# Optimization experiments

Measured on AMD Instinct MI355X. Metric: run time of the kernel, lower is better.

Reference implementation:

```python
import jax, jax.numpy as jnp
import numpy as np

B = 32
NODES = [200000, 1024, 256, 32]
CH = [1, 32, 64, 128]
EDGES = [2048000, 262144, 8192]
NCLS = 10


def _wn(V, g):
    # PyTorch weight_norm (dim=0): each output row rescaled to norm g[o]
    return g[:, None] * V / jnp.linalg.norm(V, axis=1, keepdims=True)


def _fgl(x, src, dst, n_out, W, b):
    # x: (B, C_in, N_in); sparse random-adjacency downsample then channel mix
    xt = jnp.moveaxis(x, 2, 0)                                   # (N_in, B, C_in)
    gathered = xt[src]                                           # (E, B, C_in)
    pooled = jax.ops.segment_sum(gathered, dst, num_segments=n_out)  # (N_out, B, C_in)
    return jnp.einsum('nbc,oc->bon', pooled, W) + b[None, :, None]   # (B, C_out, N_out)


def setup_inputs() -> dict:
    key = jax.random.key(0)
    ks = jax.random.split(key, 20)
    d = {}
    d['x'] = jax.random.normal(ks[0], (B, NODES[0]), jnp.float32)
    for i in range(3):
        e = EDGES[i]
        n_in, n_out = NODES[i], NODES[i + 1]
        d[f'edge_src{i}'] = jax.random.randint(ks[1 + 2 * i], (e,), 0, n_in, jnp.int32)
        d[f'edge_dst{i}'] = jnp.sort(jax.random.randint(ks[2 + 2 * i], (e,), 0, n_out, jnp.int32))
    for i in range(3):
        cin, cout = CH[i], CH[i + 1]
        d[f'V{i}'] = jax.random.normal(ks[7 + 3 * i], (cout, cin), jnp.float32) * 0.1
        d[f'g{i}'] = jnp.ones((cout,), jnp.float32)
        d[f'b{i}'] = jnp.zeros((cout,), jnp.float32)
    d['Vfc'] = jax.random.normal(ks[16], (NCLS, CH[-1] * NODES[-1]), jnp.float32) * 0.02
    d['gfc'] = jnp.ones((NCLS,), jnp.float32)
    d['bfc'] = jnp.zeros((NCLS,), jnp.float32)
    return d


def reference(x, edge_src0, edge_dst0, edge_src1, edge_dst1, edge_src2, edge_dst2,
              V0, g0, b0, V1, g1, b1, V2, g2, b2, Vfc, gfc, bfc):
    z = x[:, None, :]                                            # (B, 1, N_in)
    z = _fgl(z, edge_src0, edge_dst0, NODES[1], _wn(V0, g0), b0)  # (B, 32, 1024)
    z = _fgl(z, edge_src1, edge_dst1, NODES[2], _wn(V1, g1), b1)  # (B, 64, 256)
    z = _fgl(z, edge_src2, edge_dst2, NODES[3], _wn(V2, g2), b2)  # (B, 128, 32)
    flat = z.reshape(z.shape[0], -1)                             # (B, 4096)
    return flat @ _wn(Vfc, gfc).T + bfc                          # (B, NCLS)
```

## Files before the change

### kernel.cpp

```cpp
#include <hip/hip_runtime.h>
#include <math.h>

#define N0 200000
#define N1 1024
#define N2 256
#define N3 32
#define NE0 2048000
#define NE1 262144
#define NE2 8192
#define BATCH 32
#define NCLS 10
#define NB 4
#define SRC_PER_B 50000
#define TBLOCKS 1563
#define PREBLOCKS (N1 + TBLOCKS)

typedef _Float16 h2 __attribute__((ext_vector_type(2)));
typedef _Float16 h8 __attribute__((ext_vector_type(8)));

__device__ __forceinline__ int lower_bound_i(const int* __restrict__ a, int n, int key) {
    int lo = 0, hi = n;
    while (lo < hi) {
        int mid = (lo + hi) >> 1;
        if (a[mid] < key) lo = mid + 1; else hi = mid;
    }
    return lo;
}

__device__ __forceinline__ int wave_lower_bound(const int* __restrict__ a,
                                                int n, int key, int lane) {
    int lo = 0, hi = n;
    while (lo < hi) {
        int range = hi - lo;
        int step = (range + 63) >> 6;
        int p = lo + lane * step;
        bool ok = (p < hi) && (a[p] < key);
        unsigned long long m = __ballot(ok);
        if (m == 0ull) break;
        int L = 63 - __builtin_clzll(m);
        int nlo = lo + L * step + 1;
        int nhi = lo + (L + 1) * step;
        hi = (nhi < hi) ? nhi : hi;
        lo = nlo;
    }
    return lo;
}

__global__ __launch_bounds__(256) void k_pre(const float* __restrict__ x,
                                             h2* __restrict__ xt,
                                             const int* __restrict__ src,
                                             const int* __restrict__ dst,
                                             int* __restrict__ esrc,
                                             int* __restrict__ bstart) {
    const int i = blockIdx.x;
    const int tid = threadIdx.x;
    if (i >= N1) {
        const int t = i - N1;
        __shared__ float tile[32][129];
        const int col0 = t * 128;
        #pragma unroll
        for (int pass = 0; pass < 4; ++pass) {
            int row = (tid >> 5) + 8 * pass;
            int j4 = (tid & 31) * 4;
            int col = col0 + j4;
            if (col < N0) {
                const float4 v = *reinterpret_cast<const float4*>(&x[row * N0 + col]);
                tile[row][j4]     = v.x;
                tile[row][j4 + 1] = v.y;
                tile[row][j4 + 2] = v.z;
                tile[row][j4 + 3] = v.w;
            }
        }
        __syncthreads();
        h8* xt8 = reinterpret_cast<h8*>(xt);
        #pragma unroll
        for (int k = 0; k < 2; ++k) {
            int cl = (tid >> 2) + 64 * k;
            int col = col0 + cl;
            int c4 = tid & 3;
            if (col < N0) {
                h8 v;
                #pragma unroll
                for (int ii = 0; ii < 8; ++ii)
                    v[ii] = (_Float16)tile[8 * c4 + ii][cl];
                xt8[col * 4 + c4] = v;
            }
        }
        return;
    }
    const int n = i;
    const int wave = tid >> 6, lane = tid & 63;
    __shared__ int sB[2];
    if (wave < 2) {
        int r = wave_lower_bound(dst, NE0, n + wave, lane);
        if (lane == 0) sB[wave] = r;
    }
    __syncthreads();
    const int e0 = sB[0];
    const int e1 = sB[1];
    const int len = e1 - e0;
    const int q0 = e0 + (len * wave) / 4;
    const int q1 = e0 + (len * (wave + 1)) / 4;
    __shared__ int wcnt[4][NB];
    __shared__ int wbase[4][NB];

    int c0 = 0, c1 = 0, c2 = 0, c3 = 0;
    for (int base = q0; base < q1; base += 64) {
        int e = base + lane;
        int b = -1;
        if (e < q1) b = src[e] / SRC_PER_B;
        c0 += __popcll(__ballot(b == 0));
        c1 += __popcll(__ballot(b == 1));
        c2 += __popcll(__ballot(b == 2));
        c3 += __popcll(__ballot(b == 3));
    }
    if (lane == 0) { wcnt[wave][0] = c0; wcnt[wave][1] = c1; wcnt[wave][2] = c2; wcnt[wave][3] = c3; }
    __syncthreads();
    if (tid == 0) {
        int acc = e0;
        #pragma unroll
        for (int b = 0; b < NB; ++b) {
            bstart[n * (NB + 1) + b] = acc;
            #pragma unroll
            for (int w = 0; w < 4; ++w) { wbase[w][b] = acc; acc += wcnt[w][b]; }
        }
        bstart[n * (NB + 1) + NB] = acc;
    }
    __syncthreads();

    int u0 = wbase[wave][0], u1 = wbase[wave][1], u2 = wbase[wave][2], u3 = wbase[wave][3];
    for (int base = q0; base < q1; base += 64) {
        int e = base + lane;
        int s = 0, b = -1;
        if (e < q1) { s = src[e]; b = s / SRC_PER_B; }
        unsigned long long m0 = __ballot(b == 0);
        unsigned long long m1 = __ballot(b == 1);
        unsigned long long m2 = __ballot(b == 2);
        unsigned long long m3 = __ballot(b == 3);
        unsigned long long lt = (1ull << lane) - 1ull;
        if (b == 0)      esrc[u0 + __popcll(m0 & lt)] = s;
        else if (b == 1) esrc[u1 + __popcll(m1 & lt)] = s;
        else if (b == 2) esrc[u2 + __popcll(m2 & lt)] = s;
        else if (b == 3) esrc[u3 + __popcll(m3 & lt)] = s;
        u0 += __popcll(m0); u1 += __popcll(m1); u2 += __popcll(m2); u3 += __popcll(m3);
    }
}

__global__ __launch_bounds__(128) void k_gather0s(const h8* __restrict__ table,
                                                  const int* __restrict__ esrc,
                                                  const int* __restrict__ bstart,
                                                  _Float16* __restrict__ p0p) {
    const int b = blockIdx.x & (NB - 1);
    const int n = blockIdx.x >> 2;
    const int q0 = bstart[n * (NB + 1) + b];
    const int q1 = bstart[n * (NB + 1) + b + 1];
    const int tid = threadIdx.x;
    const int b4 = tid & 3;
    const int g  = tid >> 2;
    float acc[8] = {0.f, 0.f, 0.f, 0.f, 0.f, 0.f, 0.f, 0.f};
    int e = q0 + g;
    for (; e + 96 < q1; e += 128) {
        int s0 = esrc[e];
        int s1 = esrc[e + 32];
        int s2 = esrc[e + 64];
        int s3 = esrc[e + 96];
        h8 v0 = table[s0 * 4 + b4];
        h8 v1 = table[s1 * 4 + b4];
        h8 v2 = table[s2 * 4 + b4];
        h8 v3 = table[s3 * 4 + b4];
        #pragma unroll
        for (int i = 0; i < 8; ++i)
            acc[i] += (float)v0[i] + (float)v1[i] + (float)v2[i] + (float)v3[i];
    }
    for (; e < q1; e += 32) {
        int s = esrc[e];
        h8 v = table[s * 4 + b4];
        #pragma unroll
        for (int i = 0; i < 8; ++i) acc[i] += (float)v[i];
    }
    __shared__ float red[32][33];
    #pragma unroll
    for (int i = 0; i < 8; ++i) red[g][b4 * 8 + i] = acc[i];
    __syncthreads();
    #pragma unroll
    for (int s = 16; s >= 1; s >>= 1) {
        if (g < s) {
            #pragma unroll
            for (int i = 0; i < 8; ++i)
                red[g][b4 * 8 + i] += red[g + s][b4 * 8 + i];
        }
        __syncthreads();
    }
    if (tid < 32) p0p[(b * N1 + n) * 32 + tid] = (_Float16)red[0][tid];
}

__global__ __launch_bounds__(256) void k_gather1w(
    const h8* __restrict__ p0p, const int* __restrict__ src,
    const int* __restrict__ dst, _Float16* __restrict__ out_h,
    float* __restrict__ cnt_out,
    const float* __restrict__ V0, const float* __restrict__ g0, const float* __restrict__ b0,
    const float* __restrict__ V1, const float* __restrict__ g1, const float* __restrict__ b1,
    const float* __restrict__ V2, const float* __restrict__ g2, const float* __restrict__ b2,
    const float* __restrict__ Vfc, const float* __restrict__ gfc,
    float* __restrict__ M_, float* __restrict__ Q2_, float* __restrict__ R2_,
    float* __restrict__ B4_) {
    const int tid = threadIdx.x;
    if (blockIdx.x < N2) {
        const int n = blockIdx.x;
        const int e0 = lower_bound_i(dst, NE1, n);
        const int e1 = lower_bound_i(dst, NE1, n + 1);
        const int b4 = tid & 3;
        const int g  = tid >> 2;
        float acc[8] = {0.f, 0.f, 0.f, 0.f, 0.f, 0.f, 0.f, 0.f};
        for (int e = e0 + g; e < e1; e += 64) {
            int s = src[e];
            h8 v0 = p0p[0 * N1 * 4 + s * 4 + b4];
            h8 v1 = p0p[1 * N1 * 4 + s * 4 + b4];
            h8 v2 = p0p[2 * N1 * 4 + s * 4 + b4];
            h8 v3 = p0p[3 * N1 * 4 + s * 4 + b4];
            #pragma unroll
            for (int i = 0; i < 8; ++i)
                acc[i] += ((float)v0[i] + (float)v1[i]) + ((float)v2[i] + (float)v3[i]);
        }
        __shared__ float red[64][33];
        #pragma unroll
        for (int i = 0; i < 8; ++i) red[g][b4 * 8 + i] = acc[i];
        __syncthreads();
        #pragma unroll
        for (int s = 32; s >= 1; s >>= 1) {
            if (g < s) {
                #pragma unroll
                for (int i = 0; i < 8; ++i)
                    red[g][b4 * 8 + i] += red[g + s][b4 * 8 + i];
            }
            __syncthreads();
        }
        if (tid < 32) out_h[n * 32 + tid] = (_Float16)red[0][tid];
        else if (tid == 32) cnt_out[n] = (float)(e1 - e0);
        return;
    }
    const int k = blockIdx.x - N2;
    __shared__ float w0[32], u[64], v[64], p[128], q[128], r[128];
    __shared__ float redA[8][32], redB[8][32], redC[8][32], redD[8][32];
    __shared__ float nnred[4];
    __shared__ float scale_s;

    if (tid < 32) {
        float val = V0[tid];
        w0[tid] = g0[tid] * val / fabsf(val);
    }
    __syncthreads();
    if (tid < 64) {
        float nn = 0.f;
        #pragma unroll
        for (int c = 0; c < 32; ++c) { float t = V1[tid * 32 + c]; nn += t * t; }
        float inv = g1[tid] * rsqrtf(nn);
        float su = 0.f, sv = 0.f;
        #pragma unroll
        for (int c = 0; c < 32; ++c) {
            float w = V1[tid * 32 + c] * inv;
            su += w * w0[c]; sv += w * b0[c];
        }
        u[tid] = su; v[tid] = sv;
    }
    __syncthreads();
    if (tid < 128) {
        float nn = 0.f;
        #pragma unroll
        for (int c = 0; c < 64; ++c) { float t = V2[tid * 64 + c]; nn += t * t; }
        float inv = g2[tid] * rsqrtf(nn);
        float sp = 0.f, sq = 0.f, sr = 0.f;
        #pragma unroll
        for (int c = 0; c < 64; ++c) {
            float w = V2[tid * 64 + c] * inv;
            sp += w * u[c]; sq += w * v[c]; sr += w * b1[c];
        }
        p[tid] = sp; q[tid] = sq; r[tid] = sr;
    }
    __syncthreads();

    const int n3 = tid & 31, og = tid >> 5;
    float nn = 0.f, mk = 0.f, mq = 0.f, mr = 0.f, mb = 0.f;
    #pragma unroll
    for (int i = 0; i < 16; ++i) {
        int o = og + 8 * i;
        float w = Vfc[k * 4096 + tid + 256 * i];
        nn += w * w;
        mk += w * p[o]; mq += w * q[o]; mr += w * r[o]; mb += w * b2[o];
    }
    #pragma unroll
    for (int off = 32; off; off >>= 1) nn += __shfl_xor(nn, off);
    if ((tid & 63) == 0) nnred[tid >> 6] = nn;
    redA[og][n3] = mk; redB[og][n3] = mq; redC[og][n3] = mr; redD[og][n3] = mb;
    __syncthreads();
    if (tid == 0) {
        float s = nnred[0] + nnred[1] + nnred[2] + nnred[3];
        scale_s = gfc[k] * rsqrtf(s);
    }
    __syncthreads();
    if (tid < 32) {
        float smk = 0.f, smq = 0.f, smr = 0.f, smb = 0.f;
        #pragma unroll
        for (int i = 0; i < 8; ++i) {
            smk += redA[i][tid]; smq += redB[i][tid];
            smr += redC[i][tid]; smb += redD[i][tid];
        }
        float scale = scale_s;
        M_[k * 32 + tid]  = scale * smk;
        Q2_[k * 32 + tid] = scale * smq;
        R2_[k * 32 + tid] = scale * smr;
        float bs = scale * smb;
        #pragma unroll
        for (int off = 16; off; off >>= 1) bs += __shfl_xor(bs, off);
        if (tid == 0) B4_[k] = bs;
    }
}

__global__ __launch_bounds__(256) void k_gather2(const h8* __restrict__ table,
                                                 const int* __restrict__ src,
                                                 const int* __restrict__ dst,
                                                 const float* __restrict__ cnt_in,
                                                 float* __restrict__ out_f,
                                                 float* __restrict__ cnt_out,
                                                 float* __restrict__ t_out) {
    const int n = blockIdx.x;
    const int e0 = lower_bound_i(dst, NE2, n);
    const int e1 = lower_bound_i(dst, NE2, n + 1);
    const int tid = threadIdx.x;
    const int b4 = tid & 3;
    const int g  = tid >> 2;
    float acc[8] = {0.f, 0.f, 0.f, 0.f, 0.f, 0.f, 0.f, 0.f};
    float tacc = 0.f;
    for (int e = e0 + g; e < e1; e += 64) {
        int s = src[e];
        h8 v = table[s * 4 + b4];
        #pragma unroll
        for (int i = 0; i < 8; ++i) acc[i] += (float)v[i];
        if (b4 == 0) tacc += cnt_in[s];
    }
    __shared__ float red[64][33];
    __shared__ float tred[64];
    #pragma unroll
    for (int i = 0; i < 8; ++i) red[g][b4 * 8 + i] = acc[i];
    if (b4 == 0) tred[g] = tacc;
    __syncthreads();
    #pragma unroll
    for (int s = 32; s >= 1; s >>= 1) {
        if (g < s) {
            #pragma unroll
            for (int i = 0; i < 8; ++i)
                red[g][b4 * 8 + i] += red[g + s][b4 * 8 + i];
            if (b4 == 0) tred[g] += tred[g + s];
        }
        __syncthreads();
    }
    if (tid < 32) out_f[n * 32 + tid] = red[0][tid];
    else if (tid == 32) cnt_out[n] = (float)(e1 - e0);
    else if (tid == 33) t_out[n] = tred[0];
}

__global__ __launch_bounds__(64) void k_final(const float* __restrict__ M_,
                                              const float* __restrict__ Q2_,
                                              const float* __restrict__ R2_,
                                              const float* __restrict__ B4_,
                                              const float* __restrict__ bfc,
                                              const float* __restrict__ S2,
                                              const float* __restrict__ T2,
                                              const float* __restrict__ cnt2,
                                              float* __restrict__ out) {
    const int k = blockIdx.x;
    const int tid = threadIdx.x;
    __shared__ float Kc_s;
    float kc = 0.f;
    if (tid < 32)
        kc = Q2_[k * 32 + tid] * T2[tid] + R2_[k * 32 + tid] * cnt2[tid];
    #pragma unroll
    for (int off = 16; off; off >>= 1) kc += __shfl_xor(kc, off);
    if (tid == 0) Kc_s = kc + B4_[k] + bfc[k];
    __syncthreads();
    if (tid < 32) {
        int b = tid;
        float s = 0.f;
        #pragma unroll
        for (int n = 0; n < 32; ++n) s += M_[k * 32 + n] * S2[n * 32 + b];
        out[b * NCLS + k] = s + Kc_s;
    }
}

extern "C" void kernel_launch(void* const* d_in, const int* in_sizes, int n_in,
                              void* d_out, int out_size, void* d_ws, size_t ws_size,
                              hipStream_t stream) {
    const float* x   = (const float*)d_in[0];
    const int* src0  = (const int*)d_in[1];
    const int* dst0  = (const int*)d_in[2];
    const int* src1  = (const int*)d_in[3];
    const int* dst1  = (const int*)d_in[4];
    const int* src2  = (const int*)d_in[5];
    const int* dst2  = (const int*)d_in[6];
    const float* V0  = (const float*)d_in[7];
    const float* g0  = (const float*)d_in[8];
    const float* b0  = (const float*)d_in[9];
    const float* V1  = (const float*)d_in[10];
    const float* g1  = (const float*)d_in[11];
    const float* b1  = (const float*)d_in[12];
    const float* V2  = (const float*)d_in[13];
    const float* g2  = (const float*)d_in[14];
    const float* b2  = (const float*)d_in[15];
    const float* Vfc = (const float*)d_in[16];
    const float* gfc = (const float*)d_in[17];
    const float* bfc = (const float*)d_in[18];

    char* ws = (char*)d_ws;
    _Float16* xt   = (_Float16*)(ws);
    int* esrc      = (int*)(ws + 12800000);
    int* bstart    = (int*)(ws + 20992000);
    _Float16* P0p  = (_Float16*)(ws + 21012480);
    _Float16* S1h  = (_Float16*)(ws + 21274624);
    float* cnt1    = (float*)(ws + 21291008);
    float* S2      = (float*)(ws + 21292032);
    float* T2      = (float*)(ws + 21296128);
    float* cnt2    = (float*)(ws + 21296256);
    float* M_      = (float*)(ws + 21296384);
    float* Q2_     = (float*)(ws + 21297664);
    float* R2_     = (float*)(ws + 21298944);
    float* B4_     = (float*)(ws + 21300224);

    k_pre<<<PREBLOCKS, 256, 0, stream>>>(x, (h2*)xt, src0, dst0, esrc, bstart);
    k_gather0s<<<N1 * NB, 128, 0, stream>>>((const h8*)xt, esrc, bstart,
                                            (_Float16*)P0p);
    k_gather1w<<<N2 + NCLS, 256, 0, stream>>>((const h8*)P0p, src1, dst1,
                                              S1h, cnt1,
                                              V0, g0, b0, V1, g1, b1,
                                              V2, g2, b2, Vfc, gfc,
                                              M_, Q2_, R2_, B4_);
    k_gather2<<<N3, 256, 0, stream>>>((const h8*)S1h, src2, dst2, cnt1,
                                      S2, cnt2, T2);
    k_final<<<NCLS, 64, 0, stream>>>(M_, Q2_, R2_, B4_, bfc, S2, T2, cnt2,
                                     (float*)d_out);
}
```

Before: 65.38 us.

## Split source buckets to eight, use wave-shuffle reduction, fuse gather2 into final

The first-layer edge bucketing now splits source nodes into eight ranges instead of four. This shrinks each bucket's slice of the fp16 input table for better cache locality, and gather0 runs as single-wave blocks that reduce with shuffles instead of shared-memory tree reductions. The layer-1 gather now reads eight partial tables per source. The last-layer gather and the final classifier kernel are fused into one kernel, which drops a launch at the cost of each of the 10 blocks redundantly recomputing the small layer-2 aggregation.

```diff
diff --git a/kernel.cpp b/kernel.cpp
--- a/kernel.cpp
+++ b/kernel.cpp
@@ -10,8 +10,8 @@
 #define NE2 8192
 #define BATCH 32
 #define NCLS 10
-#define NB 4
-#define SRC_PER_B 50000
+#define NB 8
+#define SRC_PER_B 25000
 #define TBLOCKS 1563
 #define PREBLOCKS (N1 + TBLOCKS)
 
@@ -104,17 +104,21 @@
     __shared__ int wcnt[4][NB];
     __shared__ int wbase[4][NB];
 
-    int c0 = 0, c1 = 0, c2 = 0, c3 = 0;
+    int cnt[NB];
+    #pragma unroll
+    for (int b = 0; b < NB; ++b) cnt[b] = 0;
     for (int base = q0; base < q1; base += 64) {
         int e = base + lane;
         int b = -1;
         if (e < q1) b = src[e] / SRC_PER_B;
-        c0 += __popcll(__ballot(b == 0));
-        c1 += __popcll(__ballot(b == 1));
-        c2 += __popcll(__ballot(b == 2));
-        c3 += __popcll(__ballot(b == 3));
-    }
-    if (lane == 0) { wcnt[wave][0] = c0; wcnt[wave][1] = c1; wcnt[wave][2] = c2; wcnt[wave][3] = c3; }
+        #pragma unroll
+        for (int bb = 0; bb < NB; ++bb)
+            cnt[bb] += __popcll(__ballot(b == bb));
+    }
+    if (lane == 0) {
+        #pragma unroll
+        for (int b = 0; b < NB; ++b) wcnt[wave][b] = cnt[b];
+    }
     __syncthreads();
     if (tid == 0) {
         int acc = e0;
@@ -129,6 +133,7 @@
     __syncthreads();
 
     int u0 = wbase[wave][0], u1 = wbase[wave][1], u2 = wbase[wave][2], u3 = wbase[wave][3];
+    int u4 = wbase[wave][4], u5 = wbase[wave][5], u6 = wbase[wave][6], u7 = wbase[wave][7];
     for (int base = q0; base < q1; base += 64) {
         int e = base + lane;
         int s = 0, b = -1;
@@ -137,21 +142,30 @@
         unsigned long long m1 = __ballot(b == 1);
         unsigned long long m2 = __ballot(b == 2);
         unsigned long long m3 = __ballot(b == 3);
+        unsigned long long m4 = __ballot(b == 4);
+        unsigned long long m5 = __ballot(b == 5);
+        unsigned long long m6 = __ballot(b == 6);
+        unsigned long long m7 = __ballot(b == 7);
         unsigned long long lt = (1ull << lane) - 1ull;
         if (b == 0)      esrc[u0 + __popcll(m0 & lt)] = s;
         else if (b == 1) esrc[u1 + __popcll(m1 & lt)] = s;
         else if (b == 2) esrc[u2 + __popcll(m2 & lt)] = s;
         else if (b == 3) esrc[u3 + __popcll(m3 & lt)] = s;
+        else if (b == 4) esrc[u4 + __popcll(m4 & lt)] = s;
+        else if (b == 5) esrc[u5 + __popcll(m5 & lt)] = s;
+        else if (b == 6) esrc[u6 + __popcll(m6 & lt)] = s;
+        else if (b == 7) esrc[u7 + __popcll(m7 & lt)] = s;
         u0 += __popcll(m0); u1 += __popcll(m1); u2 += __popcll(m2); u3 += __popcll(m3);
-    }
-}
-
-__global__ __launch_bounds__(128) void k_gather0s(const h8* __restrict__ table,
-                                                  const int* __restrict__ esrc,
-                                                  const int* __restrict__ bstart,
-                                                  _Float16* __restrict__ p0p) {
+        u4 += __popcll(m4); u5 += __popcll(m5); u6 += __popcll(m6); u7 += __popcll(m7);
+    }
+}
+
+__global__ __launch_bounds__(64) void k_gather0s(const h8* __restrict__ table,
+                                                 const int* __restrict__ esrc,
+                                                 const int* __restrict__ bstart,
+                                                 h8* __restrict__ p0p8) {
     const int b = blockIdx.x & (NB - 1);
-    const int n = blockIdx.x >> 2;
+    const int n = blockIdx.x >> 3;
     const int q0 = bstart[n * (NB + 1) + b];
     const int q1 = bstart[n * (NB + 1) + b + 1];
     const int tid = threadIdx.x;
@@ -159,11 +173,11 @@
     const int g  = tid >> 2;
     float acc[8] = {0.f, 0.f, 0.f, 0.f, 0.f, 0.f, 0.f, 0.f};
     int e = q0 + g;
-    for (; e + 96 < q1; e += 128) {
+    for (; e + 48 < q1; e += 64) {
         int s0 = esrc[e];
-        int s1 = esrc[e + 32];
-        int s2 = esrc[e + 64];
-        int s3 = esrc[e + 96];
+        int s1 = esrc[e + 16];
+        int s2 = esrc[e + 32];
+        int s3 = esrc[e + 48];
         h8 v0 = table[s0 * 4 + b4];
         h8 v1 = table[s1 * 4 + b4];
         h8 v2 = table[s2 * 4 + b4];
@@ -172,26 +186,23 @@
         for (int i = 0; i < 8; ++i)
             acc[i] += (float)v0[i] + (float)v1[i] + (float)v2[i] + (float)v3[i];
     }
-    for (; e < q1; e += 32) {
+    for (; e < q1; e += 16) {
         int s = esrc[e];
         h8 v = table[s * 4 + b4];
         #pragma unroll
         for (int i = 0; i < 8; ++i) acc[i] += (float)v[i];
     }
-    __shared__ float red[32][33];
     #pragma unroll
-    for (int i = 0; i < 8; ++i) red[g][b4 * 8 + i] = acc[i];
-    __syncthreads();
-    #pragma unroll
-    for (int s = 16; s >= 1; s >>= 1) {
-        if (g < s) {
-            #pragma unroll
-            for (int i = 0; i < 8; ++i)
-                red[g][b4 * 8 + i] += red[g + s][b4 * 8 + i];
-        }
-        __syncthreads();
-    }
-    if (tid < 32) p0p[(b * N1 + n) * 32 + tid] = (_Float16)red[0][tid];
+    for (int o = 4; o <= 32; o <<= 1) {
+        #pragma unroll
+        for (int i = 0; i < 8; ++i) acc[i] += __shfl_xor(acc[i], o);
+    }
+    if (g == 0) {
+        h8 v;
+        #pragma unroll
+        for (int i = 0; i < 8; ++i) v[i] = (_Float16)acc[i];
+        p0p8[(b * N1 + n) * 4 + b4] = v;
+    }
 }
 
 __global__ __launch_bounds__(256) void k_gather1w(
@@ -218,9 +229,14 @@
             h8 v1 = p0p[1 * N1 * 4 + s * 4 + b4];
             h8 v2 = p0p[2 * N1 * 4 + s * 4 + b4];
             h8 v3 = p0p[3 * N1 * 4 + s * 4 + b4];
+            h8 v4 = p0p[4 * N1 * 4 + s * 4 + b4];
+            h8 v5 = p0p[5 * N1 * 4 + s * 4 + b4];
+            h8 v6 = p0p[6 * N1 * 4 + s * 4 + b4];
+            h8 v7 = p0p[7 * N1 * 4 + s * 4 + b4];
             #pragma unroll
             for (int i = 0; i < 8; ++i)
-                acc[i] += ((float)v0[i] + (float)v1[i]) + ((float)v2[i] + (float)v3[i]);
+                acc[i] += (((float)v0[i] + (float)v1[i]) + ((float)v2[i] + (float)v3[i]))
+                        + (((float)v4[i] + (float)v5[i]) + ((float)v6[i] + (float)v7[i]));
         }
         __shared__ float red[64][33];
         #pragma unroll
@@ -316,73 +332,81 @@
     }
 }
 
-__global__ __launch_bounds__(256) void k_gather2(const h8* __restrict__ table,
-                                                 const int* __restrict__ src,
-                                                 const int* __restrict__ dst,
-                                                 const float* __restrict__ cnt_in,
-                                                 float* __restrict__ out_f,
-                                                 float* __restrict__ cnt_out,
-                                                 float* __restrict__ t_out) {
-    const int n = blockIdx.x;
-    const int e0 = lower_bound_i(dst, NE2, n);
-    const int e1 = lower_bound_i(dst, NE2, n + 1);
-    const int tid = threadIdx.x;
-    const int b4 = tid & 3;
-    const int g  = tid >> 2;
-    float acc[8] = {0.f, 0.f, 0.f, 0.f, 0.f, 0.f, 0.f, 0.f};
-    float tacc = 0.f;
-    for (int e = e0 + g; e < e1; e += 64) {
-        int s = src[e];
-        h8 v = table[s * 4 + b4];
-        #pragma unroll
-        for (int i = 0; i < 8; ++i) acc[i] += (float)v[i];
-        if (b4 == 0) tacc += cnt_in[s];
-    }
-    __shared__ float red[64][33];
-    __shared__ float tred[64];
-    #pragma unroll
-    for (int i = 0; i < 8; ++i) red[g][b4 * 8 + i] = acc[i];
-    if (b4 == 0) tred[g] = tacc;
-    __syncthreads();
-    #pragma unroll
-    for (int s = 32; s >= 1; s >>= 1) {
-        if (g < s) {
-            #pragma unroll
-            for (int i = 0; i < 8; ++i)
-                red[g][b4 * 8 + i] += red[g + s][b4 * 8 + i];
-            if (b4 == 0) tred[g] += tred[g + s];
-        }
-        __syncthreads();
-    }
-    if (tid < 32) out_f[n * 32 + tid] = red[0][tid];
-    else if (tid == 32) cnt_out[n] = (float)(e1 - e0);
-    else if (tid == 33) t_out[n] = tred[0];
-}
-
-__global__ __launch_bounds__(64) void k_final(const float* __restrict__ M_,
-                                              const float* __restrict__ Q2_,
-                                              const float* __restrict__ R2_,
-                                              const float* __restrict__ B4_,
-                                              const float* __restrict__ bfc,
-                                              const float* __restrict__ S2,
-                                              const float* __restrict__ T2,
-                                              const float* __restrict__ cnt2,
-                                              float* __restrict__ out) {
+__global__ __launch_bounds__(256) void k_tail2(
+    const h8* __restrict__ tableS1, const int* __restrict__ src2,
+    const int* __restrict__ dst2, const float* __restrict__ cnt1,
+    const float* __restrict__ M_, const float* __restrict__ Q2_,
+    const float* __restrict__ R2_, const float* __restrict__ B4_,
+    const float* __restrict__ bfc, float* __restrict__ out) {
     const int k = blockIdx.x;
     const int tid = threadIdx.x;
+    __shared__ int off2_l[33];
+    __shared__ float S2_l[32][33];
+    __shared__ float T2_l[32], cnt2_l[32];
     __shared__ float Kc_s;
-    float kc = 0.f;
-    if (tid < 32)
-        kc = Q2_[k * 32 + tid] * T2[tid] + R2_[k * 32 + tid] * cnt2[tid];
+
+    if (tid < 33) off2_l[tid] = lower_bound_i(dst2, NE2, tid);
+    __syncthreads();
+
     #pragma unroll
-    for (int off = 16; off; off >>= 1) kc += __shfl_xor(kc, off);
-    if (tid == 0) Kc_s = kc + B4_[k] + bfc[k];
+    for (int pass = 0; pass < 4; ++pass) {
+        const int n = 8 * pass + (tid >> 5);
+        const int l32 = tid & 31;
+        const int b4 = l32 & 3;
+        const int g  = l32 >> 2;
+        const int e0 = off2_l[n], e1 = off2_l[n + 1];
+        float acc[8] = {0.f, 0.f, 0.f, 0.f, 0.f, 0.f, 0.f, 0.f};
+        float tacc = 0.f;
+        int e = e0 + g;
+        for (; e + 24 < e1; e += 32) {
+            int s0 = src2[e];
+            int s1 = src2[e + 8];
+            int s2 = src2[e + 16];
+            int s3 = src2[e + 24];
+            h8 v0 = tableS1[s0 * 4 + b4];
+            h8 v1 = tableS1[s1 * 4 + b4];
+            h8 v2 = tableS1[s2 * 4 + b4];
+            h8 v3 = tableS1[s3 * 4 + b4];
+            #pragma unroll
+            for (int i = 0; i < 8; ++i)
+                acc[i] += (float)v0[i] + (float)v1[i] + (float)v2[i] + (float)v3[i];
+            if (b4 == 0) tacc += cnt1[s0] + cnt1[s1] + cnt1[s2] + cnt1[s3];
+        }
+        for (; e < e1; e += 8) {
+            int s = src2[e];
+            h8 v = tableS1[s * 4 + b4];
+            #pragma unroll
+            for (int i = 0; i < 8; ++i) acc[i] += (float)v[i];
+            if (b4 == 0) tacc += cnt1[s];
+        }
+        #pragma unroll
+        for (int o = 4; o <= 16; o <<= 1) {
+            #pragma unroll
+            for (int i = 0; i < 8; ++i) acc[i] += __shfl_xor(acc[i], o);
+            tacc += __shfl_xor(tacc, o);
+        }
+        if (g == 0) {
+            #pragma unroll
+            for (int i = 0; i < 8; ++i) S2_l[n][b4 * 8 + i] = acc[i];
+            if (b4 == 0) { T2_l[n] = tacc; cnt2_l[n] = (float)(e1 - e0); }
+        }
+    }
+    __syncthreads();
+
+    {
+        float kc = 0.f;
+        if (tid < 32)
+            kc = Q2_[k * 32 + tid] * T2_l[tid] + R2_[k * 32 + tid] * cnt2_l[tid];
+        #pragma unroll
+        for (int off = 16; off; off >>= 1) kc += __shfl_xor(kc, off);
+        if (tid == 0) Kc_s = kc + B4_[k] + bfc[k];
+    }
     __syncthreads();
     if (tid < 32) {
         int b = tid;
         float s = 0.f;
         #pragma unroll
-        for (int n = 0; n < 32; ++n) s += M_[k * 32 + n] * S2[n * 32 + b];
+        for (int n = 0; n < 32; ++n) s += M_[k * 32 + n] * S2_l[n][b];
         out[b * NCLS + k] = s + Kc_s;
     }
 }
@@ -414,27 +438,22 @@
     _Float16* xt   = (_Float16*)(ws);
     int* esrc      = (int*)(ws + 12800000);
     int* bstart    = (int*)(ws + 20992000);
-    _Float16* P0p  = (_Float16*)(ws + 21012480);
-    _Float16* S1h  = (_Float16*)(ws + 21274624);
-    float* cnt1    = (float*)(ws + 21291008);
-    float* S2      = (float*)(ws + 21292032);
-    float* T2      = (float*)(ws + 21296128);
-    float* cnt2    = (float*)(ws + 21296256);
-    float* M_      = (float*)(ws + 21296384);
-    float* Q2_     = (float*)(ws + 21297664);
-    float* R2_     = (float*)(ws + 21298944);
-    float* B4_     = (float*)(ws + 21300224);
+    _Float16* P0p  = (_Float16*)(ws + 21028864);
+    _Float16* S1h  = (_Float16*)(ws + 21553152);
+    float* cnt1    = (float*)(ws + 21569536);
+    float* M_      = (float*)(ws + 21570560);
+    float* Q2_     = (float*)(ws + 21571840);
+    float* R2_     = (float*)(ws + 21573120);
+    float* B4_     = (float*)(ws + 21574400);
 
     k_pre<<<PREBLOCKS, 256, 0, stream>>>(x, (h2*)xt, src0, dst0, esrc, bstart);
-    k_gather0s<<<N1 * NB, 128, 0, stream>>>((const h8*)xt, esrc, bstart,
-                                            (_Float16*)P0p);
+    k_gather0s<<<N1 * NB, 64, 0, stream>>>((const h8*)xt, esrc, bstart,
+                                           (h8*)P0p);
     k_gather1w<<<N2 + NCLS, 256, 0, stream>>>((const h8*)P0p, src1, dst1,
                                               S1h, cnt1,
                                               V0, g0, b0, V1, g1, b1,
                                               V2, g2, b2, Vfc, gfc,
                                               M_, Q2_, R2_, B4_);
-    k_gather2<<<N3, 256, 0, stream>>>((const h8*)S1h, src2, dst2, cnt1,
-                                      S2, cnt2, T2);
-    k_final<<<NCLS, 64, 0, stream>>>(M_, Q2_, R2_, B4_, bfc, S2, T2, cnt2,
-                                     (float*)d_out);
-}
+    k_tail2<<<NCLS, 256, 0, stream>>>((const h8*)S1h, src2, dst2, cnt1,
+                                      M_, Q2_, R2_, B4_, bfc, (float*)d_out);
+}
```

New measurement: 86.17 us. 31.8% more time.
